# Optimization experiments

Measured on AMD Instinct MI355X. Metric: run time of the kernel, lower is better.

## Reference

```python
import jax, jax.numpy as jnp
import numpy as np

N = 50000   # nodes
E = 800000  # edges (avg degree 16)
K = 20      # hops per TAGConv layer
DIMS = [1, 60, 100, 200, 80, 1]  # fixed by the module


def _tagconv(x, W, b, src, dst, norm):
    """TAGConv: out = sum_{k=0..K} (A_norm^k x) @ W[k] + b.
    x: [N, Cin], W: [K+1, Cin, Cout], b: [Cout]."""
    out0 = x @ W[0] + b

    def step(carry, Wk):
        xk, acc = carry
        # one sparse propagation hop: xk <- A_norm @ xk
        xk = jax.ops.segment_sum(norm[:, None] * xk[src], dst, num_segments=N)
        return (xk, acc + xk @ Wk), None

    (_, out), _ = jax.lax.scan(step, (x, out0), W[1:])
    return out


def setup_inputs() -> dict:
    key = jax.random.key(0)
    ks = jax.random.split(key, 16)
    inp = {
        "x": jax.random.normal(ks[0], (N,), dtype=jnp.float32),
        "edge_index": jax.random.randint(ks[1], (2, E), 0, N, dtype=jnp.int32),
        "edge_weight": jax.random.uniform(ks[2], (E,), dtype=jnp.float32),
    }
    # per-layer stacked hop weights W_l: [K+1, Cin, Cout], bias b_l: [Cout]
    for l in range(5):
        cin, cout = DIMS[l], DIMS[l + 1]
        scale = 1.0 / np.sqrt(cin)
        inp[f"W{l+1}"] = jax.random.normal(ks[3 + 2 * l], (K + 1, cin, cout), dtype=jnp.float32) * scale
        inp[f"b{l+1}"] = jax.random.normal(ks[4 + 2 * l], (cout,), dtype=jnp.float32) * 0.01
    return inp


def reference(x, edge_index, edge_weight, W1, b1, W2, b2, W3, b3, W4, b4, W5, b5):
    src, dst = edge_index[0], edge_index[1]
    # gcn_norm (symmetric, no self-loops) as used by TAGConv
    deg = jax.ops.segment_sum(edge_weight, dst, num_segments=N)
    dis = jnp.where(deg > 0, jax.lax.rsqrt(jnp.where(deg > 0, deg, 1.0)), 0.0)
    norm = dis[src] * edge_weight * dis[dst]

    h = x[:, None]  # [N, 1]
    h = jax.nn.relu(_tagconv(h, W1, b1, src, dst, norm))
    h = jax.nn.relu(_tagconv(h, W2, b2, src, dst, norm))
    h = jax.nn.relu(_tagconv(h, W3, b3, src, dst, norm))
    h = jax.nn.relu(_tagconv(h, W4, b4, src, dst, norm))
    h = jax.nn.sigmoid(_tagconv(h, W5, b5, src, dst, norm))
    return jnp.squeeze(h, axis=-1)  # [N]
```

## Files before the change

kernel.cpp:

```cpp
#include <hip/hip_runtime.h>
#include <stdint.h>

#define GF_ACC    1
#define GF_BIAS   2
#define GF_RELU   8
#define GF_OBF16 16

#define BM 128
#define BN 64
#define BK 16

typedef short bf16x8 __attribute__((ext_vector_type(8)));
typedef float f32x4 __attribute__((ext_vector_type(4)));
typedef unsigned short u16x8 __attribute__((ext_vector_type(8)));

__device__ __forceinline__ float b2f(unsigned short u)
{
    return __uint_as_float(((unsigned)u) << 16);
}
__device__ __forceinline__ unsigned short f2b(float f)
{
    unsigned u = __float_as_uint(f);
    return (unsigned short)((u + 0x8000u) >> 16);
}


__global__ void deg_count_kernel(const int* __restrict__ src, const int* __restrict__ dst,
                                 const float* __restrict__ ew,
                                 float* __restrict__ deg, int* __restrict__ cnt, int E)
{
    int e = blockIdx.x * blockDim.x + threadIdx.x;
    if (e < E) {
        int d = dst[e];
        atomicAdd(&deg[d], ew[e]);
        atomicAdd(&cnt[d], 1);
    }
}

__global__ void dis_kernel(const float* __restrict__ deg, float* __restrict__ dis, int n)
{
    int i = blockIdx.x * blockDim.x + threadIdx.x;
    if (i < n) {
        float d = deg[i];
        dis[i] = (d > 0.f) ? (1.0f / sqrtf(d)) : 0.f;
    }
}

__global__ __launch_bounds__(1024) void scan_kernel(int* __restrict__ cnt_cursor,
                                                    int* __restrict__ row_ptr, int n)
{
    __shared__ int wsum[16];
    __shared__ int s_carry;
    if (threadIdx.x == 0) s_carry = 0;
    __syncthreads();
    const int VT = 8;
    const int CHUNK = 1024 * VT;
    int lane = threadIdx.x & 63;
    int wid = threadIdx.x >> 6;
    for (int base = 0; base < n; base += CHUNK) {
        int v[VT];
        int idx0 = base + threadIdx.x * VT;
        int tsum = 0;
#pragma unroll
        for (int t = 0; t < VT; t++) {
            int i = idx0 + t;
            v[t] = (i < n) ? cnt_cursor[i] : 0;
            tsum += v[t];
        }
        int incl = tsum;
        for (int off = 1; off < 64; off <<= 1) {
            int t = __shfl_up(incl, off);
            if (lane >= off) incl += t;
        }
        if (lane == 63) wsum[wid] = incl;
        __syncthreads();
        if (wid == 0) {
            int wv = (lane < 16) ? wsum[lane] : 0;
            for (int off = 1; off < 16; off <<= 1) {
                int t = __shfl_up(wv, off);
                if (lane >= off) wv += t;
            }
            if (lane < 16) wsum[lane] = wv;
        }
        __syncthreads();
        int wave_off = (wid > 0) ? wsum[wid - 1] : 0;
        int excl = incl - tsum + wave_off + s_carry;
#pragma unroll
        for (int t = 0; t < VT; t++) {
            int i = idx0 + t;
            if (i < n) {
                cnt_cursor[i] = excl;
                row_ptr[i + 1] = excl + v[t];
            }
            excl += v[t];
        }
        __syncthreads();
        if (threadIdx.x == 0) s_carry += wsum[15];
        __syncthreads();
    }
    if (threadIdx.x == 0) row_ptr[0] = 0;
}

__global__ void scatter_kernel(const int* __restrict__ src, const int* __restrict__ dst,
                               const float* __restrict__ ew, const float* __restrict__ dis,
                               int* __restrict__ cursor, int2* __restrict__ e2, int E)
{
    int e = blockIdx.x * blockDim.x + threadIdx.x;
    if (e < E) {
        int s = src[e], d = dst[e];
        int pos = atomicAdd(&cursor[d], 1);
        float nw = dis[s] * ew[e] * dis[d];
        e2[pos] = make_int2(s, __float_as_int(nw));
    }
}


__global__ __launch_bounds__(256) void prop1(const float* __restrict__ xv, const float* __restrict__ z,
                                             float* __restrict__ y, const int* __restrict__ rp,
                                             const int2* __restrict__ e2, int n, int mode)
{
    int node = blockIdx.x * 64 + (threadIdx.x >> 2);
    if (node >= n) return;
    int g = threadIdx.x & 3;
    int e0 = rp[node], e1 = rp[node + 1];
    float acc = 0.f;
    int e = e0 + g;
    for (; e + 4 < e1; e += 8) {
        int2 qa = e2[e];
        int2 qb = e2[e + 4];
        acc += __int_as_float(qa.y) * xv[qa.x];
        acc += __int_as_float(qb.y) * xv[qb.x];
    }
    if (e < e1) {
        int2 q = e2[e];
        acc += __int_as_float(q.y) * xv[q.x];
    }
    acc += __shfl_xor(acc, 1);
    acc += __shfl_xor(acc, 2);
    if (g == 0) {
        if (z) acc += z[node];
        if (mode == 1) acc = 1.0f / (1.0f + expf(-acc));
        y[node] = acc;
    }
}

template<int LPN, int CG, bool YF32, bool HASZ, bool RELU>
__global__ __launch_bounds__(256) void propw2b(const unsigned short* __restrict__ X, int xstr,
                                               const unsigned short* __restrict__ Z, int zstr,
                                               void* __restrict__ Yv, int ystr,
                                               const int* __restrict__ rp,
                                               const int2* __restrict__ e2, int n)
{
    const int NPB = 256 / LPN;
    int node = blockIdx.x * NPB + threadIdx.x / LPN;
    if (node >= n) return;
    int g = threadIdx.x % LPN;
    bool colok = (g < CG);
    int cg = colok ? g : 0;
    int e0 = rp[node], e1 = rp[node + 1];
    float acc[8] = {0.f, 0.f, 0.f, 0.f, 0.f, 0.f, 0.f, 0.f};
    int e = e0;
    if ((e & 1) && e < e1) {
        int2 q = e2[e];
        u16x8 xq = *(const u16x8*)(X + (size_t)q.x * xstr + cg * 8);
        float wv = __int_as_float(q.y);
#pragma unroll
        for (int j = 0; j < 8; j++) acc[j] += wv * b2f(xq[j]);
        e++;
    }
    for (; e + 8 <= e1; e += 8) {
        int4 p[4];
#pragma unroll
        for (int u = 0; u < 4; u++) p[u] = *(const int4*)(&e2[e + 2 * u]);
        u16x8 xq[8];
#pragma unroll
        for (int u = 0; u < 4; u++) {
            xq[2 * u]     = *(const u16x8*)(X + (size_t)p[u].x * xstr + cg * 8);
            xq[2 * u + 1] = *(const u16x8*)(X + (size_t)p[u].z * xstr + cg * 8);
        }
#pragma unroll
        for (int u = 0; u < 4; u++) {
            float w0 = __int_as_float(p[u].y);
            float w1 = __int_as_float(p[u].w);
#pragma unroll
            for (int j = 0; j < 8; j++) acc[j] += w0 * b2f(xq[2 * u][j]);
#pragma unroll
            for (int j = 0; j < 8; j++) acc[j] += w1 * b2f(xq[2 * u + 1][j]);
        }
    }
    if (e < e1) {
#pragma unroll
        for (int u = 0; u < 8; u++) {
            int eid = e + u;
            int2 q = (eid < e1) ? e2[eid] : make_int2(0, 0);
            u16x8 xq = *(const u16x8*)(X + (size_t)q.x * xstr + cg * 8);
            float wv = __int_as_float(q.y);
#pragma unroll
            for (int j = 0; j < 8; j++) acc[j] += wv * b2f(xq[j]);
        }
    }
    if (colok) {
        if (HASZ) {
            u16x8 zq = *(const u16x8*)(Z + (size_t)node * zstr + g * 8);
#pragma unroll
            for (int j = 0; j < 8; j++) acc[j] += b2f(zq[j]);
        }
        if (RELU) {
#pragma unroll
            for (int j = 0; j < 8; j++) acc[j] = fmaxf(acc[j], 0.f);
        }
        if (YF32) {
            float* Y = (float*)Yv;
            float4 lo = { acc[0], acc[1], acc[2], acc[3] };
            float4 hi = { acc[4], acc[5], acc[6], acc[7] };
            *(float4*)(Y + (size_t)node * ystr + g * 8)     = lo;
            *(float4*)(Y + (size_t)node * ystr + g * 8 + 4) = hi;
        } else {
            unsigned short* Y = (unsigned short*)Yv;
            u16x8 o;
#pragma unroll
            for (int j = 0; j < 8; j++) o[j] = f2b(acc[j]);
            *(u16x8*)(Y + (size_t)node * ystr + g * 8) = o;
        }
    }
}


__global__ __launch_bounds__(256) void gemm2(
    const float* __restrict__ X, int x_sn, int x_sk,
    const float* __restrict__ W, int w_sk, int w_sc,
    const float* __restrict__ bias,
    void* __restrict__ outv, int o_sn, int o_sc,
    int M, int K, int NC, int flags, int bias_cols)
{
    __shared__ float Xs[BK][BM + 4];
    __shared__ float Ws[BK][BN];
    int tid = threadIdx.x;
    int bm = blockIdx.x * BM;
    int bn = blockIdx.y * BN;
    int tx = tid & 15, ty = tid >> 4;
    float acc[8][4] = {};
    int xk = tid & 15, xm = tid >> 4;
    int wc = tid & 63, wk4 = tid >> 6;
    int vr = tid >> 2;
    int vc = (tid & 3) * 4;
    int wvk = tid >> 4;
    int wvc = (tid & 15) * 4;
    bool obf = (flags & GF_OBF16) != 0;
    bool xvec = (x_sk == 1) && ((x_sn & 3) == 0) && (bm + BM <= M);
    bool wvec = (w_sc == 1) && ((w_sk & 3) == 0) && (bn + BN <= NC);
    for (int k0 = 0; k0 < K; k0 += BK) {
        bool fullk = (k0 + BK <= K);
        if (xvec && fullk) {
#pragma unroll
            for (int h = 0; h < 2; h++) {
                int m = vr + 64 * h;
                const float4 q = *(const float4*)(X + (size_t)(bm + m) * x_sn + k0 + vc);
                Xs[vc + 0][m] = q.x; Xs[vc + 1][m] = q.y;
                Xs[vc + 2][m] = q.z; Xs[vc + 3][m] = q.w;
            }
        } else {
#pragma unroll
            for (int r = 0; r < 8; r++) {
                int m = xm + 16 * r;
                int gm = bm + m, gk = k0 + xk;
                Xs[xk][m] = (gm < M && gk < K) ? X[(size_t)gm * x_sn + (size_t)gk * x_sk] : 0.f;
            }
        }
        if (wvec && fullk) {
            *(float4*)&Ws[wvk][wvc] = *(const float4*)(W + (size_t)(k0 + wvk) * w_sk + bn + wvc);
        } else {
#pragma unroll
            for (int r = 0; r < 4; r++) {
                int kk = wk4 + 4 * r;
                int gk = k0 + kk, gc = bn + wc;
                Ws[kk][wc] = (gk < K && gc < NC) ? W[(size_t)gk * w_sk + (size_t)gc * w_sc] : 0.f;
            }
        }
        __syncthreads();
#pragma unroll
        for (int kk = 0; kk < BK; kk++) {
            float xv[8], wv[4];
#pragma unroll
            for (int i = 0; i < 8; i++) xv[i] = Xs[kk][ty * 8 + i];
#pragma unroll
            for (int j = 0; j < 4; j++) wv[j] = Ws[kk][tx * 4 + j];
#pragma unroll
            for (int i = 0; i < 8; i++)
#pragma unroll
                for (int j = 0; j < 4; j++)
                    acc[i][j] += xv[i] * wv[j];
        }
        __syncthreads();
    }
    bool ovec = !obf && (o_sc == 1) && ((o_sn & 3) == 0) && (bn + tx * 4 + 3 < NC);
#pragma unroll
    for (int i = 0; i < 8; i++) {
        int gm = bm + ty * 8 + i;
        if (gm >= M) continue;
        if (ovec) {
            float* op = (float*)outv + (size_t)gm * o_sn + bn + tx * 4;
            float4 v = { acc[i][0], acc[i][1], acc[i][2], acc[i][3] };
            if (flags & GF_ACC) {
                float4 o = *(const float4*)op;
                v.x += o.x; v.y += o.y; v.z += o.z; v.w += o.w;
            }
            if (flags & GF_BIAS) {
#pragma unroll
                for (int j = 0; j < 4; j++) {
                    int gc = bn + tx * 4 + j;
                    if (gc < bias_cols) (&v.x)[j] += bias[gc];
                }
            }
            if (flags & GF_RELU) {
                v.x = fmaxf(v.x, 0.f); v.y = fmaxf(v.y, 0.f);
                v.z = fmaxf(v.z, 0.f); v.w = fmaxf(v.w, 0.f);
            }
            *(float4*)op = v;
        } else {
#pragma unroll
            for (int j = 0; j < 4; j++) {
                int gc = bn + tx * 4 + j;
                if (gc >= NC) continue;
                size_t oi = (size_t)gm * o_sn + (size_t)gc * o_sc;
                float v = acc[i][j];
                if (obf) {
                    unsigned short* o = (unsigned short*)outv;
                    if (flags & GF_ACC)  v += b2f(o[oi]);
                    if ((flags & GF_BIAS) && gc < bias_cols) v += bias[gc];
                    if (flags & GF_RELU) v = fmaxf(v, 0.f);
                    o[oi] = f2b(v);
                } else {
                    float* o = (float*)outv;
                    if (flags & GF_ACC)  v += o[oi];
                    if ((flags & GF_BIAS) && gc < bias_cols) v += bias[gc];
                    if (flags & GF_RELU) v = fmaxf(v, 0.f);
                    o[oi] = v;
                }
            }
        }
    }
}


__device__ __forceinline__ void bf16_split2(float v, unsigned short* h,
                                            unsigned short* l)
{
    unsigned u = __float_as_uint(v);
    unsigned uh = (u + 0x8000u) & 0xFFFF0000u;
    float r1 = v - __uint_as_float(uh);
    unsigned ul = (__float_as_uint(r1) + 0x8000u) & 0xFFFF0000u;
    *h = (unsigned short)(uh >> 16);
    *l = (unsigned short)(ul >> 16);
}

__global__ void splitW_stack(const float* __restrict__ Wsrc, int hop0, int H,
                             int Cin, int Cout, int slot, int Kpad, int NCpad,
                             unsigned short* __restrict__ hi, unsigned short* __restrict__ lo)
{
    int t = blockIdx.x * blockDim.x + threadIdx.x;
    if (t >= NCpad * Kpad) return;
    int k = t % Kpad, n = t / Kpad;
    int j = k / slot, c = k % slot;
    float v = (n < Cout && j < H && c < Cin)
        ? Wsrc[((size_t)(hop0 + j) * Cin + c) * Cout + n] : 0.f;
    unsigned short h8, l8;
    bf16_split2(v, &h8, &l8);
    hi[t] = h8; lo[t] = l8;
}

__global__ void splitW_horner(const float* __restrict__ W4, int k_lo, int nb,
                              int Kpad, int NCpad,
                              unsigned short* __restrict__ hi, unsigned short* __restrict__ lo)
{
    int t = blockIdx.x * blockDim.x + threadIdx.x;
    if (t >= NCpad * Kpad) return;
    int k = t % Kpad, n = t / Kpad;
    float v = 0.f;
    if (k < 200 && n < nb * 80) {
        int hop = k_lo + n / 80, co = n % 80;
        v = W4[(size_t)hop * 16000 + (size_t)k * 80 + co];
    }
    unsigned short h8, l8;
    bf16_split2(v, &h8, &l8);
    hi[t] = h8; lo[t] = l8;
}

#define MFM 128
#define MFN 128
#define ASTU 40

__global__ __launch_bounds__(512) void gemm_mfma(
    const unsigned short* __restrict__ X, int x_sn,
    const unsigned short* __restrict__ Whi, const unsigned short* __restrict__ Wlo,
    int Kpad,
    const float* __restrict__ bias,
    void* __restrict__ outv, int o_sn,
    int M, int NC, int flags, int bias_cols)
{
    __shared__ unsigned short Af[MFM][ASTU];
    __shared__ unsigned short Bh[MFN][ASTU];
    __shared__ unsigned short Bl[MFN][ASTU];
    int tid = threadIdx.x;
    int bm = blockIdx.x * MFM;
    int bn = blockIdx.y * MFN;
    int w = tid >> 6, lane = tid & 63;
    int q = lane >> 4, r = lane & 15;
    f32x4 acc[8];
#pragma unroll
    for (int b = 0; b < 8; b++)
        acc[b] = (f32x4){0.f, 0.f, 0.f, 0.f};
    int sm = tid >> 2;
    int skq = (tid & 3) * 8;
    const unsigned short* xbase = X + (size_t)(bm + sm) * x_sn + skq;
    int ksteps = Kpad / 32;
    for (int ks = 0; ks < ksteps; ks++) {
        int k0 = ks * 32;
        *(u16x8*)&Af[sm][skq] = *(const u16x8*)(xbase + k0);
        size_t wo = (size_t)(bn + sm) * Kpad + k0 + skq;
        *(u16x8*)&Bh[sm][skq] = *(const u16x8*)(Whi + wo);
        *(u16x8*)&Bl[sm][skq] = *(const u16x8*)(Wlo + wo);
        __syncthreads();
        {
            bf16x8 a = *(const bf16x8*)&Af[w * 16 + r][q * 8];
#pragma unroll
            for (int nt = 0; nt < 8; nt++) {
                bf16x8 bh = *(const bf16x8*)&Bh[nt * 16 + r][q * 8];
                bf16x8 bl = *(const bf16x8*)&Bl[nt * 16 + r][q * 8];
                acc[nt] = __builtin_amdgcn_mfma_f32_16x16x32_bf16(a, bl, acc[nt], 0, 0, 0);
                acc[nt] = __builtin_amdgcn_mfma_f32_16x16x32_bf16(a, bh, acc[nt], 0, 0, 0);
            }
        }
        __syncthreads();
    }
    bool obf = (flags & GF_OBF16) != 0;
#pragma unroll
    for (int i = 0; i < 4; i++) {
        int gm = bm + w * 16 + q * 4 + i;
        if (gm >= M) continue;
#pragma unroll
        for (int nt = 0; nt < 8; nt++) {
            int gc = bn + nt * 16 + r;
            if (gc >= NC) continue;
            size_t oi = (size_t)gm * o_sn + gc;
            float v = acc[nt][i];
            if (obf) {
                unsigned short* o = (unsigned short*)outv;
                if (flags & GF_ACC)  v += b2f(o[oi]);
                if ((flags & GF_BIAS) && gc < bias_cols) v += bias[gc];
                if (flags & GF_RELU) v = fmaxf(v, 0.f);
                o[oi] = f2b(v);
            } else {
                float* o = (float*)outv;
                if (flags & GF_ACC)  v += o[oi];
                if ((flags & GF_BIAS) && gc < bias_cols) v += bias[gc];
                if (flags & GF_RELU) v = fmaxf(v, 0.f);
                o[oi] = v;
            }
        }
    }
}


extern "C" void kernel_launch(void* const* d_in, const int* in_sizes, int n_in,
                              void* d_out, int out_size, void* d_ws, size_t ws_size,
                              hipStream_t stream)
{
    const int N = 50000, E = 800000, K = 20;
    const float* x  = (const float*)d_in[0];
    const int*   ei = (const int*)d_in[1];
    const float* ew = (const float*)d_in[2];
    const float* Wl[5]; const float* bl[5];
    for (int l = 0; l < 5; l++) { Wl[l] = (const float*)d_in[3 + 2 * l]; bl[l] = (const float*)d_in[4 + 2 * l]; }
    const int* src = ei;
    const int* dst = ei + E;
    (void)in_sizes; (void)n_in; (void)out_size;

    uintptr_t base = (uintptr_t)d_ws;
    uintptr_t cur = base;
    auto alloc = [&](size_t bytes) -> char* {
        uintptr_t q = (cur + 255) & ~(uintptr_t)255;
        cur = q + bytes;
        return (char*)q;
    };
    float* deg    = (float*)alloc((size_t)N * 4);
    float* dis    = (float*)alloc((size_t)N * 4);
    int*   rowptr = (int*)alloc((size_t)(N + 1) * 4);
    int*   cursor = (int*)alloc((size_t)N * 4);
    int2*  e2     = (int2*)alloc((size_t)E * 8);
    float* Zb     = (float*)alloc((size_t)(K + 1) * N * 4);
    float* ya     = (float*)alloc((size_t)N * 4);
    float* yb     = (float*)alloc((size_t)N * 4);
    size_t h1e = (size_t)N * 64  + 8192;
    size_t h2e = (size_t)N * 104 + 8192;
    size_t h3e = (size_t)N * 200 + 8192;
    unsigned short* h1 = (unsigned short*)alloc(h1e * 2);
    unsigned short* h2 = (unsigned short*)alloc(h2e * 2);
    unsigned short* h3 = (unsigned short*)alloc(h3e * 2);
    float*          h4 = (float*)alloc((size_t)N * 80 * 4);
    unsigned short* Ra = (unsigned short*)alloc((size_t)N * 96 * 2);
    unsigned short* Rb = (unsigned short*)alloc((size_t)N * 96 * 2);

    size_t used = (size_t)(cur - base);
    size_t reserve = (size_t)8 << 20;
    size_t avail = (ws_size > used + reserve) ? (ws_size - used - reserve) : 0;
    size_t cap = (size_t)N * 2000 * 4;
    size_t arena_bytes = avail < cap ? avail : cap;
    unsigned short* Sb = (unsigned short*)alloc(arena_bytes);
    unsigned short* WThi = (unsigned short*)alloc((size_t)2 << 20);
    unsigned short* WTlo = (unsigned short*)alloc((size_t)2 << 20);
    const size_t cacheCap = (size_t)128 << 20;
    size_t lim = arena_bytes < cacheCap ? arena_bytes : cacheCap;
    auto clampH = [&](int slotw, int hi) {
        long h = (long)(lim / ((size_t)N * slotw * 2));
        if (h < 1) h = 1;
        if (h > hi) h = hi;
        return (int)h;
    };
    const int H2s = clampH(64, K);
    const int H3s = clampH(104, K);
    const int B4s = clampH(80, K + 1);
    const int rowstr2u = H2s * 64;
    const int rowstr3u = H3s * 104;
    const int rowstr4u = B4s * 80;

    hipMemsetAsync(deg, 0, (size_t)N * 4, stream);
    hipMemsetAsync(cursor, 0, (size_t)N * 4, stream);
    hipMemsetAsync(h1, 0, h1e * 2, stream);
    hipMemsetAsync(h2, 0, h2e * 2, stream);
    hipMemsetAsync(h3, 0, h3e * 2, stream);
    deg_count_kernel<<<(E + 255) / 256, 256, 0, stream>>>(src, dst, ew, deg, cursor, E);
    dis_kernel<<<(N + 255) / 256, 256, 0, stream>>>(deg, dis, N);
    scan_kernel<<<1, 1024, 0, stream>>>(cursor, rowptr, N);
    scatter_kernel<<<(E + 255) / 256, 256, 0, stream>>>(src, dst, ew, dis, cursor, e2, E);

    const int PB  = (N + 63) / 64;
    const int PB8 = (N + 31) / 32;
    const int P16 = (N + 15) / 16;
    const int GMX = (N + BM - 1) / BM;
    const int MGX = (N + MFM - 1) / MFM;
    auto gyf = [](int NC) { return (NC + BN - 1) / BN; };

    hipMemcpyAsync(Zb, x, (size_t)N * 4, hipMemcpyDeviceToDevice, stream);
    for (int k = 1; k <= K; k++)
        prop1<<<PB, 256, 0, stream>>>(Zb + (size_t)(k - 1) * N, nullptr, Zb + (size_t)k * N,
                                      rowptr, e2, N, 0);
    gemm2<<<dim3(GMX, gyf(60)), 256, 0, stream>>>(Zb, 1, N, Wl[0], 60, 1, bl[0],
                                                  h1, 64, 1, N, K + 1, 60,
                                                  GF_BIAS | GF_RELU | GF_OBF16, 60);

    splitW_stack<<<(128 * 64 + 255) / 256, 256, 0, stream>>>(Wl[1], 0, 1, 60, 100, 64,
                                                             64, 128, WThi, WTlo);
    gemm_mfma<<<dim3(MGX, 1), 512, 0, stream>>>(h1, 64, WThi, WTlo, 64,
        bl[1], h2, 104, N, 100, GF_BIAS | GF_OBF16, 100);
    {
        int done = 0;
        const unsigned short* prevp = h1; int prevstr = 64;
        while (done < K) {
            int H = (K - done < H2s) ? (K - done) : H2s;
            for (int j = 0; j < H; j++) {
                unsigned short* dstp = Sb + j * 64;
                propw2b<8, 8, false, false, false><<<PB8, 256, 0, stream>>>(prevp, prevstr,
                    nullptr, 0, dstp, rowstr2u, rowptr, e2, N);
                prevp = dstp; prevstr = rowstr2u;
            }
            int Kg = H * 64;
            int tot = 128 * Kg;
            splitW_stack<<<(tot + 255) / 256, 256, 0, stream>>>(Wl[1], 1 + done, H, 60, 100, 64,
                                                               Kg, 128, WThi, WTlo);
            bool last = (done + H == K);
            gemm_mfma<<<dim3(MGX, 1), 512, 0, stream>>>(Sb, rowstr2u, WThi, WTlo, Kg,
                nullptr, h2, 104, N, 100, GF_ACC | GF_OBF16 | (last ? GF_RELU : 0), 0);
            done += H;
        }
    }

    splitW_stack<<<(256 * 128 + 255) / 256, 256, 0, stream>>>(Wl[2], 0, 1, 100, 200, 128,
                                                              128, 256, WThi, WTlo);
    gemm_mfma<<<dim3(MGX, 2), 512, 0, stream>>>(h2, 104, WThi, WTlo, 128,
        bl[2], h3, 200, N, 200, GF_BIAS | GF_OBF16, 200);
    {
        int done = 0;
        const unsigned short* prevp = h2; int prevstr = 104;
        while (done < K) {
            int H = (K - done < H3s) ? (K - done) : H3s;
            for (int j = 0; j < H; j++) {
                unsigned short* dstp = Sb + j * 104;
                propw2b<16, 13, false, false, false><<<P16, 256, 0, stream>>>(prevp, prevstr,
                    nullptr, 0, dstp, rowstr3u, rowptr, e2, N);
                prevp = dstp; prevstr = rowstr3u;
            }
            int Kg = H * 104;
            int Kp = (Kg + 31) & ~31;
            int tot = 256 * Kp;
            splitW_stack<<<(tot + 255) / 256, 256, 0, stream>>>(Wl[2], 1 + done, H, 100, 200, 104,
                                                               Kp, 256, WThi, WTlo);
            bool last = (done + H == K);
            gemm_mfma<<<dim3(MGX, 2), 512, 0, stream>>>(Sb, rowstr3u, WThi, WTlo, Kp,
                nullptr, h3, 200, N, 200, GF_ACC | GF_OBF16 | (last ? GF_RELU : 0), 0);
            done += H;
        }
    }

    {
        const unsigned short* curR = nullptr; int curstr = 0;
        int k_hi = K;
        while (k_hi >= 0) {
            int k_lo = k_hi - B4s + 1; if (k_lo < 0) k_lo = 0;
            int nb = k_hi - k_lo + 1;
            int NCp = ((nb * 80 + 127) / 128) * 128;
            int tot = NCp * 224;
            splitW_horner<<<(tot + 255) / 256, 256, 0, stream>>>(Wl[3], k_lo, nb, 224, NCp,
                                                                 WThi, WTlo);
            gemm_mfma<<<dim3(MGX, NCp / 128), 512, 0, stream>>>(h3, 200, WThi, WTlo, 224,
                bl[3], Sb, rowstr4u, N, nb * 80, (k_lo == 0 ? GF_BIAS : 0) | GF_OBF16, 80);
            int kstart;
            if (k_hi == K) { curR = Sb + (size_t)(K - k_lo) * 80; curstr = rowstr4u; kstart = K - 1; }
            else kstart = k_hi;
            for (int k = kstart; k >= k_lo; k--) {
                const unsigned short* Zp = Sb + (size_t)(k - k_lo) * 80;
                if (k == 0) {
                    propw2b<16, 10, true, true, true><<<P16, 256, 0, stream>>>(curR, curstr,
                        Zp, rowstr4u, h4, 80, rowptr, e2, N);
                } else {
                    unsigned short* o = (k & 1) ? Ra : Rb;
                    propw2b<16, 10, false, true, false><<<P16, 256, 0, stream>>>(curR, curstr,
                        Zp, rowstr4u, o, 96, rowptr, e2, N);
                    curR = o; curstr = 96;
                }
            }
            k_hi = k_lo - 1;
        }
    }

    gemm2<<<dim3(GMX, gyf(21)), 256, 0, stream>>>(h4, 80, 1, Wl[4], 1, 80, bl[4],
                                                  Zb, 1, N, N, 80, K + 1, GF_BIAS, 1);
    const float* cur5 = Zb + (size_t)K * N;
    float* outp = (float*)d_out;
    for (int k = K - 1; k >= 0; k--) {
        float* o = (k == 0) ? outp : ((k & 1) ? ya : yb);
        prop1<<<PB, 256, 0, stream>>>(cur5, Zb + (size_t)k * N, o,
                                      rowptr, e2, N, (k == 0) ? 1 : 0);
        cur5 = o;
    }
}
```

Measured before the change: 2.879 ms.

## Pack propagation lanes exactly per node and retile MFMA GEMM warps 2x4

The sparse propagation kernel now takes a columns-per-lane template parameter, so each node uses exactly as many lanes as its feature width needs (4x16, 13x8, 5x16) instead of padding to 8 or 16 lanes with idle ones. More nodes fit per block and fewer threads are wasted. The MFMA GEMM changes each warp from a 16x128 tile to a 64x32 tile, so A and B fragment loads from shared memory are reused across more MFMAs. The risks are higher register pressure from wider per-lane accumulators, and 13- or 5-lane node groups that straddle wavefronts and leave some threads idle per block.

```diff
diff --git a/kernel.cpp b/kernel.cpp
--- a/kernel.cpp
+++ b/kernel.cpp
@@ -144,7 +144,7 @@
     }
 }
 
-template<int LPN, int CG, bool YF32, bool HASZ, bool RELU>
+template<int LPN, int CPL, bool YF32, bool HASZ, bool RELU>
 __global__ __launch_bounds__(256) void propw2b(const unsigned short* __restrict__ X, int xstr,
                                                const unsigned short* __restrict__ Z, int zstr,
                                                void* __restrict__ Yv, int ystr,
@@ -152,75 +152,102 @@
                                                const int2* __restrict__ e2, int n)
 {
     const int NPB = 256 / LPN;
-    int node = blockIdx.x * NPB + threadIdx.x / LPN;
+    const int NC8 = CPL * 8;
+    int nid = threadIdx.x / LPN;
+    if (nid >= NPB) return;
+    int node = blockIdx.x * NPB + nid;
     if (node >= n) return;
     int g = threadIdx.x % LPN;
-    bool colok = (g < CG);
-    int cg = colok ? g : 0;
     int e0 = rp[node], e1 = rp[node + 1];
-    float acc[8] = {0.f, 0.f, 0.f, 0.f, 0.f, 0.f, 0.f, 0.f};
+    float acc[NC8];
+#pragma unroll
+    for (int j = 0; j < NC8; j++) acc[j] = 0.f;
+    const unsigned short* xcol = X + g * NC8;
     int e = e0;
     if ((e & 1) && e < e1) {
         int2 q = e2[e];
-        u16x8 xq = *(const u16x8*)(X + (size_t)q.x * xstr + cg * 8);
         float wv = __int_as_float(q.y);
 #pragma unroll
-        for (int j = 0; j < 8; j++) acc[j] += wv * b2f(xq[j]);
+        for (int c = 0; c < CPL; c++) {
+            u16x8 xq = *(const u16x8*)(xcol + (size_t)q.x * xstr + c * 8);
+#pragma unroll
+            for (int j = 0; j < 8; j++) acc[c * 8 + j] += wv * b2f(xq[j]);
+        }
         e++;
     }
-    for (; e + 8 <= e1; e += 8) {
-        int4 p[4];
-#pragma unroll
-        for (int u = 0; u < 4; u++) p[u] = *(const int4*)(&e2[e + 2 * u]);
-        u16x8 xq[8];
-#pragma unroll
-        for (int u = 0; u < 4; u++) {
-            xq[2 * u]     = *(const u16x8*)(X + (size_t)p[u].x * xstr + cg * 8);
-            xq[2 * u + 1] = *(const u16x8*)(X + (size_t)p[u].z * xstr + cg * 8);
-        }
-#pragma unroll
-        for (int u = 0; u < 4; u++) {
+    const int UN = (CPL == 2) ? 4 : 8;
+    for (; e + UN <= e1; e += UN) {
+        int4 p[UN / 2];
+#pragma unroll
+        for (int u = 0; u < UN / 2; u++) p[u] = *(const int4*)(&e2[e + 2 * u]);
+        u16x8 xq[UN][CPL];
+#pragma unroll
+        for (int u = 0; u < UN / 2; u++) {
+#pragma unroll
+            for (int c = 0; c < CPL; c++) {
+                xq[2 * u][c]     = *(const u16x8*)(xcol + (size_t)p[u].x * xstr + c * 8);
+                xq[2 * u + 1][c] = *(const u16x8*)(xcol + (size_t)p[u].z * xstr + c * 8);
+            }
+        }
+#pragma unroll
+        for (int u = 0; u < UN / 2; u++) {
             float w0 = __int_as_float(p[u].y);
             float w1 = __int_as_float(p[u].w);
 #pragma unroll
-            for (int j = 0; j < 8; j++) acc[j] += w0 * b2f(xq[2 * u][j]);
-#pragma unroll
-            for (int j = 0; j < 8; j++) acc[j] += w1 * b2f(xq[2 * u + 1][j]);
+            for (int c = 0; c < CPL; c++)
+#pragma unroll
+                for (int j = 0; j < 8; j++) acc[c * 8 + j] += w0 * b2f(xq[2 * u][c][j]);
+#pragma unroll
+            for (int c = 0; c < CPL; c++)
+#pragma unroll
+                for (int j = 0; j < 8; j++) acc[c * 8 + j] += w1 * b2f(xq[2 * u + 1][c][j]);
         }
     }
     if (e < e1) {
 #pragma unroll
-        for (int u = 0; u < 8; u++) {
+        for (int u = 0; u < UN; u++) {
             int eid = e + u;
             int2 q = (eid < e1) ? e2[eid] : make_int2(0, 0);
-            u16x8 xq = *(const u16x8*)(X + (size_t)q.x * xstr + cg * 8);
             float wv = __int_as_float(q.y);
 #pragma unroll
-            for (int j = 0; j < 8; j++) acc[j] += wv * b2f(xq[j]);
-        }
-    }
-    if (colok) {
+            for (int c = 0; c < CPL; c++) {
+                u16x8 xq = *(const u16x8*)(xcol + (size_t)q.x * xstr + c * 8);
+#pragma unroll
+                for (int j = 0; j < 8; j++) acc[c * 8 + j] += wv * b2f(xq[j]);
+            }
+        }
+    }
+    {
         if (HASZ) {
-            u16x8 zq = *(const u16x8*)(Z + (size_t)node * zstr + g * 8);
-#pragma unroll
-            for (int j = 0; j < 8; j++) acc[j] += b2f(zq[j]);
+#pragma unroll
+            for (int c = 0; c < CPL; c++) {
+                u16x8 zq = *(const u16x8*)(Z + (size_t)node * zstr + g * NC8 + c * 8);
+#pragma unroll
+                for (int j = 0; j < 8; j++) acc[c * 8 + j] += b2f(zq[j]);
+            }
         }
         if (RELU) {
 #pragma unroll
-            for (int j = 0; j < 8; j++) acc[j] = fmaxf(acc[j], 0.f);
+            for (int j = 0; j < NC8; j++) acc[j] = fmaxf(acc[j], 0.f);
         }
         if (YF32) {
-            float* Y = (float*)Yv;
-            float4 lo = { acc[0], acc[1], acc[2], acc[3] };
-            float4 hi = { acc[4], acc[5], acc[6], acc[7] };
-            *(float4*)(Y + (size_t)node * ystr + g * 8)     = lo;
-            *(float4*)(Y + (size_t)node * ystr + g * 8 + 4) = hi;
+            float* Y = (float*)Yv + (size_t)node * ystr + g * NC8;
+#pragma unroll
+            for (int c = 0; c < CPL; c++) {
+                float4 lo = { acc[c * 8 + 0], acc[c * 8 + 1], acc[c * 8 + 2], acc[c * 8 + 3] };
+                float4 hi = { acc[c * 8 + 4], acc[c * 8 + 5], acc[c * 8 + 6], acc[c * 8 + 7] };
+                *(float4*)(Y + c * 8)     = lo;
+                *(float4*)(Y + c * 8 + 4) = hi;
+            }
         } else {
-            unsigned short* Y = (unsigned short*)Yv;
-            u16x8 o;
-#pragma unroll
-            for (int j = 0; j < 8; j++) o[j] = f2b(acc[j]);
-            *(u16x8*)(Y + (size_t)node * ystr + g * 8) = o;
+            unsigned short* Y = (unsigned short*)Yv + (size_t)node * ystr + g * NC8;
+#pragma unroll
+            for (int c = 0; c < CPL; c++) {
+                u16x8 o;
+#pragma unroll
+                for (int j = 0; j < 8; j++) o[j] = f2b(acc[c * 8 + j]);
+                *(u16x8*)(Y + c * 8) = o;
+            }
         }
     }
 }
@@ -405,11 +432,14 @@
     int bm = blockIdx.x * MFM;
     int bn = blockIdx.y * MFN;
     int w = tid >> 6, lane = tid & 63;
+    int wm = w & 1, wn = w >> 1;
     int q = lane >> 4, r = lane & 15;
-    f32x4 acc[8];
-#pragma unroll
-    for (int b = 0; b < 8; b++)
-        acc[b] = (f32x4){0.f, 0.f, 0.f, 0.f};
+    f32x4 acc[4][2];
+#pragma unroll
+    for (int a = 0; a < 4; a++)
+#pragma unroll
+        for (int b = 0; b < 2; b++)
+            acc[a][b] = (f32x4){0.f, 0.f, 0.f, 0.f};
     int sm = tid >> 2;
     int skq = (tid & 3) * 8;
     const unsigned short* xbase = X + (size_t)(bm + sm) * x_sn + skq;
@@ -422,40 +452,51 @@
         *(u16x8*)&Bl[sm][skq] = *(const u16x8*)(Wlo + wo);
         __syncthreads();
         {
-            bf16x8 a = *(const bf16x8*)&Af[w * 16 + r][q * 8];
-#pragma unroll
-            for (int nt = 0; nt < 8; nt++) {
-                bf16x8 bh = *(const bf16x8*)&Bh[nt * 16 + r][q * 8];
-                bf16x8 bl = *(const bf16x8*)&Bl[nt * 16 + r][q * 8];
-                acc[nt] = __builtin_amdgcn_mfma_f32_16x16x32_bf16(a, bl, acc[nt], 0, 0, 0);
-                acc[nt] = __builtin_amdgcn_mfma_f32_16x16x32_bf16(a, bh, acc[nt], 0, 0, 0);
-            }
+            bf16x8 a[4], bh[2], bl2[2];
+#pragma unroll
+            for (int mt = 0; mt < 4; mt++)
+                a[mt] = *(const bf16x8*)&Af[wm * 64 + mt * 16 + r][q * 8];
+#pragma unroll
+            for (int nl = 0; nl < 2; nl++) {
+                bh[nl]  = *(const bf16x8*)&Bh[wn * 32 + nl * 16 + r][q * 8];
+                bl2[nl] = *(const bf16x8*)&Bl[wn * 32 + nl * 16 + r][q * 8];
+            }
+#pragma unroll
+            for (int mt = 0; mt < 4; mt++)
+#pragma unroll
+                for (int nl = 0; nl < 2; nl++) {
+                    acc[mt][nl] = __builtin_amdgcn_mfma_f32_16x16x32_bf16(a[mt], bl2[nl], acc[mt][nl], 0, 0, 0);
+                    acc[mt][nl] = __builtin_amdgcn_mfma_f32_16x16x32_bf16(a[mt], bh[nl],  acc[mt][nl], 0, 0, 0);
+                }
         }
         __syncthreads();
     }
     bool obf = (flags & GF_OBF16) != 0;
 #pragma unroll
-    for (int i = 0; i < 4; i++) {
-        int gm = bm + w * 16 + q * 4 + i;
-        if (gm >= M) continue;
-#pragma unroll
-        for (int nt = 0; nt < 8; nt++) {
-            int gc = bn + nt * 16 + r;
-            if (gc >= NC) continue;
-            size_t oi = (size_t)gm * o_sn + gc;
-            float v = acc[nt][i];
-            if (obf) {
-                unsigned short* o = (unsigned short*)outv;
-                if (flags & GF_ACC)  v += b2f(o[oi]);
-                if ((flags & GF_BIAS) && gc < bias_cols) v += bias[gc];
-                if (flags & GF_RELU) v = fmaxf(v, 0.f);
-                o[oi] = f2b(v);
-            } else {
-                float* o = (float*)outv;
-                if (flags & GF_ACC)  v += o[oi];
-                if ((flags & GF_BIAS) && gc < bias_cols) v += bias[gc];
-                if (flags & GF_RELU) v = fmaxf(v, 0.f);
-                o[oi] = v;
+    for (int mt = 0; mt < 4; mt++) {
+#pragma unroll
+        for (int i = 0; i < 4; i++) {
+            int gm = bm + wm * 64 + mt * 16 + q * 4 + i;
+            if (gm >= M) continue;
+#pragma unroll
+            for (int nl = 0; nl < 2; nl++) {
+                int gc = bn + wn * 32 + nl * 16 + r;
+                if (gc >= NC) continue;
+                size_t oi = (size_t)gm * o_sn + gc;
+                float v = acc[mt][nl][i];
+                if (obf) {
+                    unsigned short* o = (unsigned short*)outv;
+                    if (flags & GF_ACC)  v += b2f(o[oi]);
+                    if ((flags & GF_BIAS) && gc < bias_cols) v += bias[gc];
+                    if (flags & GF_RELU) v = fmaxf(v, 0.f);
+                    o[oi] = f2b(v);
+                } else {
+                    float* o = (float*)outv;
+                    if (flags & GF_ACC)  v += o[oi];
+                    if ((flags & GF_BIAS) && gc < bias_cols) v += bias[gc];
+                    if (flags & GF_RELU) v = fmaxf(v, 0.f);
+                    o[oi] = v;
+                }
             }
         }
     }
@@ -535,8 +576,9 @@
     scatter_kernel<<<(E + 255) / 256, 256, 0, stream>>>(src, dst, ew, dis, cursor, e2, E);
 
     const int PB  = (N + 63) / 64;
-    const int PB8 = (N + 31) / 32;
-    const int P16 = (N + 15) / 16;
+    const int PL2 = (N + 63) / 64;
+    const int PL3 = (N + 18) / 19;
+    const int PL4 = (N + 50) / 51;
     const int GMX = (N + BM - 1) / BM;
     const int MGX = (N + MFM - 1) / MFM;
     auto gyf = [](int NC) { return (NC + BN - 1) / BN; };
@@ -560,7 +602,7 @@
             int H = (K - done < H2s) ? (K - done) : H2s;
             for (int j = 0; j < H; j++) {
                 unsigned short* dstp = Sb + j * 64;
-                propw2b<8, 8, false, false, false><<<PB8, 256, 0, stream>>>(prevp, prevstr,
+                propw2b<4, 2, false, false, false><<<PL2, 256, 0, stream>>>(prevp, prevstr,
                     nullptr, 0, dstp, rowstr2u, rowptr, e2, N);
                 prevp = dstp; prevstr = rowstr2u;
             }
@@ -586,7 +628,7 @@
             int H = (K - done < H3s) ? (K - done) : H3s;
             for (int j = 0; j < H; j++) {
                 unsigned short* dstp = Sb + j * 104;
-                propw2b<16, 13, false, false, false><<<P16, 256, 0, stream>>>(prevp, prevstr,
+                propw2b<13, 1, false, false, false><<<PL3, 256, 0, stream>>>(prevp, prevstr,
                     nullptr, 0, dstp, rowstr3u, rowptr, e2, N);
                 prevp = dstp; prevstr = rowstr3u;
             }
@@ -620,11 +662,11 @@
             for (int k = kstart; k >= k_lo; k--) {
                 const unsigned short* Zp = Sb + (size_t)(k - k_lo) * 80;
                 if (k == 0) {
-                    propw2b<16, 10, true, true, true><<<P16, 256, 0, stream>>>(curR, curstr,
+                    propw2b<5, 2, true, true, true><<<PL4, 256, 0, stream>>>(curR, curstr,
                         Zp, rowstr4u, h4, 80, rowptr, e2, N);
                 } else {
                     unsigned short* o = (k & 1) ? Ra : Rb;
-                    propw2b<16, 10, false, true, false><<<P16, 256, 0, stream>>>(curR, curstr,
+                    propw2b<5, 2, false, true, false><<<PL4, 256, 0, stream>>>(curR, curstr,
                         Zp, rowstr4u, o, 96, rowptr, e2, N);
                     curR = o; curstr = 96;
                 }
```

After: 2.744 ms, median of 2. 1.05x faster.
